# Optimization experiments

Measured on AMD Instinct MI355X. Metric: run time of the kernel, lower is better.

The kernel has to match this reference:

```python
import jax, jax.numpy as jnp
import numpy as np


def gcn_conv(x, src, dst, W, b, n_nodes):
    """PyG GCNConv: out = D^-1/2 (A+I) D^-1/2 (x @ W) + b.
    src/dst already include self loops. Shapes: x [N,F], src/dst [E+N].
    """
    h = x @ W  # [N, H] - linear transform first (PyG order)
    # symmetric normalization from (unweighted) degree of A + I
    deg = jax.ops.segment_sum(jnp.ones_like(dst, dtype=h.dtype), dst,
                              num_segments=n_nodes)  # [N]
    dis = jnp.where(deg > 0, jax.lax.rsqrt(deg), 0.0)  # deg_inv_sqrt, inf->0
    norm = dis[src] * dis[dst]  # [E+N]
    msg = h[src] * norm[:, None]  # gather + scale  [E+N, H]
    out = jax.ops.segment_sum(msg, dst, num_segments=n_nodes)  # scatter-add
    return out + b


def setup_inputs() -> dict:
    key = jax.random.key(0)
    ks = jax.random.split(key, 4)
    N, E, F, H, C = 50000, 1600000, 768, 128, 2
    x = jax.random.normal(ks[0], (N, F), dtype=jnp.float32)
    edge_index = jax.random.randint(ks[1], (2, E), 0, N, dtype=jnp.int64)
    W1 = jax.random.normal(ks[2], (F, H), dtype=jnp.float32) * (1.0 / np.sqrt(F))
    b1 = jnp.zeros((H,), dtype=jnp.float32)
    W2 = jax.random.normal(ks[3], (H, C), dtype=jnp.float32) * (1.0 / np.sqrt(H))
    b2 = jnp.zeros((C,), dtype=jnp.float32)
    return {"x": x, "edge_index": edge_index, "W1": W1, "b1": b1,
            "W2": W2, "b2": b2}


def reference(x, edge_index, W1, b1, W2, b2):
    n_nodes = x.shape[0]
    # add self loops once (PyG GCNConv default add_self_loops=True)
    loops = jnp.arange(n_nodes, dtype=edge_index.dtype)
    src = jnp.concatenate([edge_index[0], loops])
    dst = jnp.concatenate([edge_index[1], loops])
    h = jax.nn.relu(gcn_conv(x, src, dst, W1, b1, n_nodes))
    h = gcn_conv(h, src, dst, W2, b2, n_nodes)
    return jax.nn.softmax(h, axis=-1)
```

## Files before the change

### kernel.cpp

```cpp
#include <hip/hip_runtime.h>
#include <hip/hip_bf16.h>
#include <stdint.h>

#define F_IN 768
#define H_DIM 128
#define CAP 128

typedef __attribute__((ext_vector_type(8))) short short8;
typedef __attribute__((ext_vector_type(4))) float floatx4;

__device__ __forceinline__ unsigned short f2bf(float f) {
    union { float f; unsigned u; } v; v.f = f;
    unsigned r = v.u + 0x7fff + ((v.u >> 16) & 1);
    return (unsigned short)(r >> 16);
}
__device__ __forceinline__ float bflo(unsigned u) {
    union { unsigned u; float f; } v; v.u = u << 16;
    return v.f;
}
__device__ __forceinline__ float bfhi(unsigned u) {
    union { unsigned u; float f; } v; v.u = u & 0xffff0000u;
    return v.f;
}

__global__ void k_init(int* __restrict__ cnt, int N,
                       const float* __restrict__ W1, unsigned short* __restrict__ W1B) {
    int t = blockIdx.x * blockDim.x + threadIdx.x;
    if (t < N) cnt[t] = 0;
    if (t < 8 * 24 * 64) {
        int lane = t & 63;
        int kb = (t >> 6) % 24;
        int f  = (t >> 6) / 24;
        int r = lane & 15, quad = lane >> 4;
        int col = f * 16 + r;
        int k0 = kb * 32 + quad * 8;
        unsigned short* o = W1B + (size_t)t * 8;
#pragma unroll
        for (int j = 0; j < 8; j++) o[j] = f2bf(W1[(size_t)(k0 + j) * H_DIM + col]);
    }
}

__global__ __launch_bounds__(256) void k_build(const int* __restrict__ ei, int E, int N,
                                               int* __restrict__ cnt, int* __restrict__ csr) {
    int g = blockIdx.x & 7;
    int r = blockIdx.x >> 3;
    int nbg = gridDim.x >> 3;
    int span = (N + 7) >> 3;
    int lo = g * span, hi = min(lo + span, N);
    for (int e = r * 256 + threadIdx.x; e < E; e += nbg * 256) {
        int d = ei[E + e];
        d = min(max(d, 0), N - 1);
        if (d >= lo && d < hi) {
            int s = ei[e];
            s = min(max(s, 0), N - 1);
            int pos = atomicAdd(&cnt[d], 1);
            if (pos < CAP) csr[(size_t)d * CAP + pos] = s;
        }
    }
}

__global__ void k_dis(const int* __restrict__ cnt, float* __restrict__ dis, int N) {
    int i = blockIdx.x * blockDim.x + threadIdx.x;
    if (i < N) dis[i] = rsqrtf((float)(cnt[i] + 1));
}

#define CH 256
#define S_CH 268

#define LOADC(c)                                                         \
    { _Pragma("unroll")                                                  \
      for (int j = 0; j < 8; j++)                                        \
          v[j] = *(const floatx4*)(rp[j] + (c) * CH); }

#define STOREC(b)                                                        \
    { _Pragma("unroll")                                                  \
      for (int j = 0; j < 8; j++) {                                      \
          uint2 w;                                                       \
          w.x = (unsigned)f2bf(v[j][0]) | ((unsigned)f2bf(v[j][1]) << 16); \
          w.y = (unsigned)f2bf(v[j][2]) | ((unsigned)f2bf(v[j][3]) << 16); \
          *(uint2*)(&As[b][(4 * j + wv) * S_CH + (lane << 2)]) = w; } }

#define MFMAC(b, c)                                                      \
    { _Pragma("unroll")                                                  \
      for (int kb = 0; kb < 8; kb++) {                                   \
          short8 af0 = *(const short8*)(&As[b][r * S_CH + quad * 8 + kb * 32]);        \
          short8 af1 = *(const short8*)(&As[b][(16 + r) * S_CH + quad * 8 + kb * 32]); \
          short8 b0 = *(const short8*)(bp + ((c) * 8 + kb) * 512);       \
          short8 b1 = *(const short8*)(bp + 12288 + ((c) * 8 + kb) * 512); \
          acc00 = __builtin_amdgcn_mfma_f32_16x16x32_bf16(af0, b0, acc00, 0, 0, 0); \
          acc01 = __builtin_amdgcn_mfma_f32_16x16x32_bf16(af0, b1, acc01, 0, 0, 0); \
          acc10 = __builtin_amdgcn_mfma_f32_16x16x32_bf16(af1, b0, acc10, 0, 0, 0); \
          acc11 = __builtin_amdgcn_mfma_f32_16x16x32_bf16(af1, b1, acc11, 0, 0, 0); } }

__global__ __launch_bounds__(256) void k_gemm1(const float* __restrict__ x,
                                               const unsigned short* __restrict__ W1B,
                                               unsigned short* __restrict__ h, int N) {
    __shared__ unsigned short As[2][32 * S_CH];
    int rowblk = blockIdx.x * 32;
    int tid = threadIdx.x;
    int wv = tid >> 6;
    int lane = tid & 63;
    int quad = lane >> 4;
    int r = lane & 15;

    const float* rp[8];
#pragma unroll
    for (int j = 0; j < 8; j++) {
        int sr = min(rowblk + 4 * j + wv, N - 1);
        rp[j] = x + (size_t)sr * F_IN + (lane << 2);
    }

    const unsigned short* bp = W1B + ((size_t)(2 * wv) * 24 * 512) + (size_t)lane * 8;

    floatx4 acc00 = (floatx4){0.f, 0.f, 0.f, 0.f};
    floatx4 acc01 = (floatx4){0.f, 0.f, 0.f, 0.f};
    floatx4 acc10 = (floatx4){0.f, 0.f, 0.f, 0.f};
    floatx4 acc11 = (floatx4){0.f, 0.f, 0.f, 0.f};

    floatx4 v[8];

    LOADC(0);
    STOREC(0);
    __syncthreads();

    LOADC(1);
    MFMAC(0, 0);
    STOREC(1);
    __syncthreads();

    LOADC(2);
    MFMAC(1, 1);
    STOREC(0);
    __syncthreads();

    MFMAC(0, 2);

    int c0 = (2 * wv) * 16 + r, c1 = (2 * wv + 1) * 16 + r;
#pragma unroll
    for (int i = 0; i < 4; i++) {
        int orow0 = rowblk + quad * 4 + i;
        int orow1 = orow0 + 16;
        if (orow0 < N) {
            h[(size_t)orow0 * H_DIM + c0] = f2bf(acc00[i]);
            h[(size_t)orow0 * H_DIM + c1] = f2bf(acc01[i]);
        }
        if (orow1 < N) {
            h[(size_t)orow1 * H_DIM + c0] = f2bf(acc10[i]);
            h[(size_t)orow1 * H_DIM + c1] = f2bf(acc11[i]);
        }
    }
}

__global__ __launch_bounds__(256) void k_agg1(const unsigned short* __restrict__ h,
                                              const int* __restrict__ csr,
                                              const int* __restrict__ cnt,
                                              const float* __restrict__ dis,
                                              const float* __restrict__ b1,
                                              const float* __restrict__ W2,
                                              float* __restrict__ h2, int N) {
    int wv = (blockIdx.x * blockDim.x + threadIdx.x) >> 6;
    if (wv >= N) return;
    int lane = threadIdx.x & 63;
    int c = lane & 15;
    int p = lane >> 4;
    int nedge = min(cnt[wv], CAP);
    int beg = wv * CAP;
    float dv = dis[wv];

    uint4 hs = *(const uint4*)(h + (size_t)wv * H_DIM + 8 * c);
    float sf = (p == 0) ? dv : 0.f;
    float a0 = sf * bflo(hs.x), a1 = sf * bfhi(hs.x);
    float a2 = sf * bflo(hs.y), a3 = sf * bfhi(hs.y);
    float a4 = sf * bflo(hs.z), a5 = sf * bfhi(hs.z);
    float a6 = sf * bflo(hs.w), a7 = sf * bfhi(hs.w);

    for (int j0 = 0; j0 < nedge; j0 += 64) {
        int idx = j0 + lane;
        bool valid = idx < nedge;
        int u = csr[valid ? (beg + idx) : beg];
        float du = valid ? dis[u] : 0.f;
        int cnt64 = nedge - j0; if (cnt64 > 64) cnt64 = 64;
        int quads = (cnt64 + 3) >> 2;
        for (int t = 0; t < quads; t++) {
            int srcl = 4 * t + p;
            int uu = __shfl(u, srcl);
            float dd = __shfl(du, srcl);
            uint4 hv = *(const uint4*)(h + (size_t)uu * H_DIM + 8 * c);
            a0 += dd * bflo(hv.x); a1 += dd * bfhi(hv.x);
            a2 += dd * bflo(hv.y); a3 += dd * bfhi(hv.y);
            a4 += dd * bflo(hv.z); a5 += dd * bfhi(hv.z);
            a6 += dd * bflo(hv.w); a7 += dd * bfhi(hv.w);
        }
    }
    a0 += __shfl_xor(a0, 16); a0 += __shfl_xor(a0, 32);
    a1 += __shfl_xor(a1, 16); a1 += __shfl_xor(a1, 32);
    a2 += __shfl_xor(a2, 16); a2 += __shfl_xor(a2, 32);
    a3 += __shfl_xor(a3, 16); a3 += __shfl_xor(a3, 32);
    a4 += __shfl_xor(a4, 16); a4 += __shfl_xor(a4, 32);
    a5 += __shfl_xor(a5, 16); a5 += __shfl_xor(a5, 32);
    a6 += __shfl_xor(a6, 16); a6 += __shfl_xor(a6, 32);
    a7 += __shfl_xor(a7, 16); a7 += __shfl_xor(a7, 32);

    floatx4 bb0 = *(const floatx4*)(b1 + 8 * c);
    floatx4 bb1 = *(const floatx4*)(b1 + 8 * c + 4);
    float h0 = fmaxf(a0 * dv + bb0[0], 0.f);
    float h1 = fmaxf(a1 * dv + bb0[1], 0.f);
    float h2a = fmaxf(a2 * dv + bb0[2], 0.f);
    float h3 = fmaxf(a3 * dv + bb0[3], 0.f);
    float h4 = fmaxf(a4 * dv + bb1[0], 0.f);
    float h5 = fmaxf(a5 * dv + bb1[1], 0.f);
    float h6 = fmaxf(a6 * dv + bb1[2], 0.f);
    float h7 = fmaxf(a7 * dv + bb1[3], 0.f);
    const float* w2p = W2 + 16 * c;
    floatx4 wA = *(const floatx4*)(w2p);
    floatx4 wB = *(const floatx4*)(w2p + 4);
    floatx4 wC = *(const floatx4*)(w2p + 8);
    floatx4 wD = *(const floatx4*)(w2p + 12);
    float p0 = h0 * wA[0] + h1 * wA[2] + h2a * wB[0] + h3 * wB[2]
             + h4 * wC[0] + h5 * wC[2] + h6 * wD[0] + h7 * wD[2];
    float p1 = h0 * wA[1] + h1 * wA[3] + h2a * wB[1] + h3 * wB[3]
             + h4 * wC[1] + h5 * wC[3] + h6 * wD[1] + h7 * wD[3];
#pragma unroll
    for (int m = 8; m >= 1; m >>= 1) {
        p0 += __shfl_xor(p0, m);
        p1 += __shfl_xor(p1, m);
    }
    if (lane == 0) {
        h2[(size_t)wv * 2]     = p0;
        h2[(size_t)wv * 2 + 1] = p1;
    }
}

__global__ __launch_bounds__(256) void k_agg2sm(const int* __restrict__ csr,
                                                const int* __restrict__ cnt,
                                                const float* __restrict__ dis,
                                                const float* __restrict__ h2,
                                                const float* __restrict__ b2,
                                                float* __restrict__ out, int N) {
    int i = (blockIdx.x * blockDim.x + threadIdx.x) >> 4;
    if (i >= N) return;
    int l = threadIdx.x & 15;
    int nedge = min(cnt[i], CAP);
    int beg = i * CAP;
    float dv = dis[i];
    float2 hself = *(const float2*)(h2 + (size_t)i * 2);
    float sf = (l == 0) ? dv : 0.f;
    float a0 = sf * hself.x, a1 = sf * hself.y;
    for (int j = l; j < nedge; j += 16) {
        int u = csr[beg + j];
        float w = dis[u];
        float2 hv = *(const float2*)(h2 + (size_t)u * 2);
        a0 += w * hv.x;
        a1 += w * hv.y;
    }
#pragma unroll
    for (int m = 8; m >= 1; m >>= 1) {
        a0 += __shfl_xor(a0, m);
        a1 += __shfl_xor(a1, m);
    }
    if (l == 0) {
        float o0 = a0 * dv + b2[0];
        float o1 = a1 * dv + b2[1];
        float m = fmaxf(o0, o1);
        float e0 = __expf(o0 - m), e1 = __expf(o1 - m);
        float inv = 1.f / (e0 + e1);
        float2 r; r.x = e0 * inv; r.y = e1 * inv;
        *(float2*)(out + (size_t)i * 2) = r;
    }
}

extern "C" void kernel_launch(void* const* d_in, const int* in_sizes, int n_in,
                              void* d_out, int out_size, void* d_ws, size_t ws_size,
                              hipStream_t stream) {
    const float* x  = (const float*)d_in[0];
    const int*   ei = (const int*)d_in[1];
    const float* W1 = (const float*)d_in[2];
    const float* b1 = (const float*)d_in[3];
    const float* W2 = (const float*)d_in[4];
    const float* b2 = (const float*)d_in[5];
    int N = in_sizes[0] / F_IN;
    int E = in_sizes[1] / 2;

    char* p = (char*)d_ws;
    auto alloc = [&](size_t bytes) {
        void* q = (void*)p;
        p += (bytes + 255) & ~(size_t)255;
        return q;
    };
    int* cnt              = (int*)alloc((size_t)N * 4);
    int* csr              = (int*)alloc((size_t)N * CAP * 4);
    float* dis            = (float*)alloc((size_t)N * 4);
    unsigned short* W1B   = (unsigned short*)alloc((size_t)F_IN * H_DIM * 2);
    unsigned short* h     = (unsigned short*)alloc((size_t)N * H_DIM * 2);
    float* h2             = (float*)alloc((size_t)N * 2 * 4);
    float* out            = (float*)d_out;

    k_init<<<(N + 255) / 256, 256, 0, stream>>>(cnt, N, W1, W1B);
    k_build<<<2048, 256, 0, stream>>>(ei, E, N, cnt, csr);
    k_dis<<<(N + 255) / 256, 256, 0, stream>>>(cnt, dis, N);
    k_gemm1<<<(N + 31) / 32, 256, 0, stream>>>(x, W1B, h, N);
    k_agg1<<<(N + 3) / 4, 256, 0, stream>>>(h, csr, cnt, dis, b1, W2, h2, N);
    k_agg2sm<<<(N * 16 + 255) / 256, 256, 0, stream>>>(csr, cnt, dis, h2, b2, out, N);
}
```

Measured before the change: 392.0 us.

## Split GEMM1 K-loop into six smaller chunks with deeper register prefetch

The first-layer GEMM now stages the 768-wide input in six 128-column chunks instead of three 256-column chunks. Loads for up to three chunks are kept in flight in registers while the MFMAs run on LDS double buffers. Occupancy is hinted at 3 blocks per CU, and the LDS footprint per block is halved. This aims to hide global-load latency on the streaming x read. The cost is more barriers and more register pressure.

```diff
diff --git a/kernel.cpp b/kernel.cpp
--- a/kernel.cpp
+++ b/kernel.cpp
@@ -64,38 +64,39 @@
     if (i < N) dis[i] = rsqrtf((float)(cnt[i] + 1));
 }
 
-#define CH 256
-#define S_CH 268
-
-#define LOADC(c)                                                         \
+#define CH6 128
+#define S6 140
+
+#define LOAD6(vv, c)                                                     \
     { _Pragma("unroll")                                                  \
-      for (int j = 0; j < 8; j++)                                        \
-          v[j] = *(const floatx4*)(rp[j] + (c) * CH); }
-
-#define STOREC(b)                                                        \
+      for (int j = 0; j < 4; j++)                                        \
+          vv[j] = *(const floatx4*)(rp[j] + (c) * CH6); }
+
+#define STORE6(b, vv)                                                    \
     { _Pragma("unroll")                                                  \
-      for (int j = 0; j < 8; j++) {                                      \
+      for (int j = 0; j < 4; j++) {                                      \
           uint2 w;                                                       \
-          w.x = (unsigned)f2bf(v[j][0]) | ((unsigned)f2bf(v[j][1]) << 16); \
-          w.y = (unsigned)f2bf(v[j][2]) | ((unsigned)f2bf(v[j][3]) << 16); \
-          *(uint2*)(&As[b][(4 * j + wv) * S_CH + (lane << 2)]) = w; } }
-
-#define MFMAC(b, c)                                                      \
+          w.x = (unsigned)f2bf(vv[j][0]) | ((unsigned)f2bf(vv[j][1]) << 16); \
+          w.y = (unsigned)f2bf(vv[j][2]) | ((unsigned)f2bf(vv[j][3]) << 16); \
+          *(uint2*)(&As[b][woff[j]]) = w; } }
+
+#define MFMA6(b, c)                                                      \
     { _Pragma("unroll")                                                  \
-      for (int kb = 0; kb < 8; kb++) {                                   \
-          short8 af0 = *(const short8*)(&As[b][r * S_CH + quad * 8 + kb * 32]);        \
-          short8 af1 = *(const short8*)(&As[b][(16 + r) * S_CH + quad * 8 + kb * 32]); \
-          short8 b0 = *(const short8*)(bp + ((c) * 8 + kb) * 512);       \
-          short8 b1 = *(const short8*)(bp + 12288 + ((c) * 8 + kb) * 512); \
+      for (int kk = 0; kk < 4; kk++) {                                   \
+          short8 af0 = *(const short8*)(&As[b][r * S6 + kk * 32 + quad * 8]);        \
+          short8 af1 = *(const short8*)(&As[b][(16 + r) * S6 + kk * 32 + quad * 8]); \
+          int kbg = (c) * 4 + kk;                                        \
+          short8 b0 = *(const short8*)(bp + kbg * 512);                  \
+          short8 b1 = *(const short8*)(bp + 12288 + kbg * 512);          \
           acc00 = __builtin_amdgcn_mfma_f32_16x16x32_bf16(af0, b0, acc00, 0, 0, 0); \
           acc01 = __builtin_amdgcn_mfma_f32_16x16x32_bf16(af0, b1, acc01, 0, 0, 0); \
           acc10 = __builtin_amdgcn_mfma_f32_16x16x32_bf16(af1, b0, acc10, 0, 0, 0); \
           acc11 = __builtin_amdgcn_mfma_f32_16x16x32_bf16(af1, b1, acc11, 0, 0, 0); } }
 
-__global__ __launch_bounds__(256) void k_gemm1(const float* __restrict__ x,
-                                               const unsigned short* __restrict__ W1B,
-                                               unsigned short* __restrict__ h, int N) {
-    __shared__ unsigned short As[2][32 * S_CH];
+__global__ __launch_bounds__(256, 3) void k_gemm1(const float* __restrict__ x,
+                                                  const unsigned short* __restrict__ W1B,
+                                                  unsigned short* __restrict__ h, int N) {
+    __shared__ unsigned short As[2][32 * S6];
     int rowblk = blockIdx.x * 32;
     int tid = threadIdx.x;
     int wv = tid >> 6;
@@ -103,11 +104,15 @@
     int quad = lane >> 4;
     int r = lane & 15;
 
-    const float* rp[8];
-#pragma unroll
-    for (int j = 0; j < 8; j++) {
-        int sr = min(rowblk + 4 * j + wv, N - 1);
-        rp[j] = x + (size_t)sr * F_IN + (lane << 2);
+    const float* rp[4];
+    int woff[4];
+#pragma unroll
+    for (int j = 0; j < 4; j++) {
+        int idx = j * 256 + tid;
+        int row = idx >> 5, c4 = idx & 31;
+        int sr = min(rowblk + row, N - 1);
+        rp[j] = x + (size_t)sr * F_IN + c4 * 4;
+        woff[j] = row * S6 + c4 * 4;
     }
 
     const unsigned short* bp = W1B + ((size_t)(2 * wv) * 24 * 512) + (size_t)lane * 8;
@@ -117,23 +122,18 @@
     floatx4 acc10 = (floatx4){0.f, 0.f, 0.f, 0.f};
     floatx4 acc11 = (floatx4){0.f, 0.f, 0.f, 0.f};
 
-    floatx4 v[8];
-
-    LOADC(0);
-    STOREC(0);
+    floatx4 v0[4], v1[4], v2[4];
+
+    LOAD6(v0, 0); LOAD6(v1, 1); LOAD6(v2, 2);
+    STORE6(0, v0);
     __syncthreads();
 
-    LOADC(1);
-    MFMAC(0, 0);
-    STOREC(1);
-    __syncthreads();
-
-    LOADC(2);
-    MFMAC(1, 1);
-    STOREC(0);
-    __syncthreads();
-
-    MFMAC(0, 2);
+    LOAD6(v0, 3); MFMA6(0, 0); STORE6(1, v1); __syncthreads();
+    LOAD6(v1, 4); MFMA6(1, 1); STORE6(0, v2); __syncthreads();
+    LOAD6(v2, 5); MFMA6(0, 2); STORE6(1, v0); __syncthreads();
+    MFMA6(1, 3); STORE6(0, v1); __syncthreads();
+    MFMA6(0, 4); STORE6(1, v2); __syncthreads();
+    MFMA6(1, 5);
 
     int c0 = (2 * wv) * 16 + r, c1 = (2 * wv + 1) * 16 + r;
 #pragma unroll
```

Measured after the change: 393.2 us. No clear change (+0.3%).
